# Optimization experiments

Hardware: AMD Instinct MI355X
Metric: run time of the kernel (lower is better)

## Reference

```python
import jax, jax.numpy as jnp
import numpy as np

N_NODES = 100000
N_EDGES = 1600000
D_IN = 128
D_HID = 128
D_OUT = 64
N_LAYERS = 3
BN_EPS = 1e-5


def _mlp_block(h, W1, b1, g, be, W2, b2):
    # PyG MLP([c_in, h, h]): Linear -> BatchNorm -> ReLU -> Linear (plain last)
    h = h @ W1 + b1                      # [N, h]
    mu = jnp.mean(h, axis=0)
    var = jnp.var(h, axis=0)             # biased var, BN training-mode stats
    h = (h - mu) * jax.lax.rsqrt(var + BN_EPS) * g + be
    h = jax.nn.relu(h)
    return h @ W2 + b2


def setup_inputs() -> dict:
    key = jax.random.key(0)
    ks = jax.random.split(key, 16)
    s_in = 1.0 / np.sqrt(D_IN)
    s_h = 1.0 / np.sqrt(D_HID)
    x = jax.random.normal(ks[0], (N_NODES, D_IN), dtype=jnp.float32)
    edge_index = jax.random.randint(ks[1], (2, N_EDGES), 0, N_NODES, dtype=jnp.int64)
    return {
        "x": x,
        "edge_index": edge_index,
        # stacked per-conv MLP params (all layers are 128->128->128)
        "W1": jax.random.normal(ks[2], (N_LAYERS, D_IN, D_HID), jnp.float32) * s_in,
        "b1": jnp.zeros((N_LAYERS, D_HID), jnp.float32),
        "g1": jnp.ones((N_LAYERS, D_HID), jnp.float32),
        "be1": jnp.zeros((N_LAYERS, D_HID), jnp.float32),
        "W2": jax.random.normal(ks[3], (N_LAYERS, D_HID, D_HID), jnp.float32) * s_h,
        "b2": jnp.zeros((N_LAYERS, D_HID), jnp.float32),
        # final MLP([h, h, out])
        "fW1": jax.random.normal(ks[4], (D_HID, D_HID), jnp.float32) * s_h,
        "fb1": jnp.zeros((D_HID,), jnp.float32),
        "fg1": jnp.ones((D_HID,), jnp.float32),
        "fbe1": jnp.zeros((D_HID,), jnp.float32),
        "fW2": jax.random.normal(ks[5], (D_HID, D_OUT), jnp.float32) * s_h,
        "fb2": jnp.zeros((D_OUT,), jnp.float32),
    }


def reference(x, edge_index, W1, b1, g1, be1, W2, b2, fW1, fb1, fg1, fbe1, fW2, fb2):
    src, dst = edge_index[0], edge_index[1]
    for l in range(N_LAYERS):
        # GINConv, eps=0: nn((1+eps)*x + sum_{j->i} x_j)
        aggr = jax.ops.segment_sum(x[src], dst, num_segments=N_NODES)  # [N, d]
        h = x + aggr
        x = jax.nn.relu(_mlp_block(h, W1[l], b1[l], g1[l], be1[l], W2[l], b2[l]))
    # final MLP (dropout=0.5 is identity in eval mode)
    return _mlp_block(x, fW1, fb1, fg1, fbe1, fW2, fb2)
```

## Files before the change

kernel.cpp:

```cpp
#include <hip/hip_runtime.h>

#define NN 100000
#define NE 1600000
#define DD 128
#define CAP 56
#define NGROUP 256

static __device__ __forceinline__ unsigned short f2b(float f) {
  unsigned int x = __float_as_uint(f);
  unsigned int r = x + 0x7fffu + ((x >> 16) & 1u);
  return (unsigned short)(r >> 16);
}
static __device__ __forceinline__ float b2f(unsigned short u) {
  return __uint_as_float(((unsigned int)u) << 16);
}

typedef __attribute__((ext_vector_type(8))) short short8;
typedef __attribute__((ext_vector_type(4))) float f32x4;

union V8 {
  uint4 u4;
  short8 s8;
  unsigned short us[8];
};

__global__ void detect_k(const int* __restrict__ ei, int* __restrict__ flag) {
  int v = ei[2 * threadIdx.x + 1];
  unsigned long long b = __ballot(v != 0);
  if (threadIdx.x == 0) *flag = (b == 0ull) ? 1 : 0;
}

__global__ __launch_bounds__(256) void cast_k(const float* __restrict__ x,
                                              unsigned short* __restrict__ x16) {
  size_t i = ((size_t)blockIdx.x * 256 + threadIdx.x) * 8;
  f32x4 a = *(const f32x4*)(x + i);
  f32x4 b = *(const f32x4*)(x + i + 4);
  V8 v;
#pragma unroll
  for (int j = 0; j < 4; ++j) {
    v.us[j] = f2b(a[j]);
    v.us[4 + j] = f2b(b[j]);
  }
  *(uint4*)(x16 + i) = v.u4;
}

__global__ __launch_bounds__(256) void pack_k(const int* __restrict__ ei,
                                              int2* __restrict__ packed,
                                              int* __restrict__ cnt,
                                              const int* __restrict__ flag) {
  const int mode = *flag;
  const int gid = blockIdx.x * 256 + threadIdx.x;
  int s, d;
  if (mode) {
    s = ((const int2*)ei)[gid].x;
    d = ((const int2*)ei)[(size_t)NE + gid].x;
  } else {
    s = ei[gid];
    d = ei[NE + gid];
  }
  packed[gid] = make_int2(s, d);
  if (gid < NN) cnt[gid] = 0;
}

__global__ __launch_bounds__(256) void scatter_k(const int2* __restrict__ packed,
                                                 int* __restrict__ cnt,
                                                 int* __restrict__ csr) {
  const int r = blockIdx.x & 7;
  const int g = blockIdx.x >> 3;
  const int lo = r * (NN / 8), hi = lo + (NN / 8);
  for (int e = g * 256 + threadIdx.x; e < NE; e += NGROUP * 256) {
    int2 sd = packed[e];
    if (sd.y >= lo && sd.y < hi) {
      int c = atomicAdd(&cnt[sd.y], 1);
      if (c < CAP) csr[(size_t)sd.y * CAP + c] = sd.x;
    }
  }
}

__global__ __launch_bounds__(256) void wprep_k(const float* __restrict__ W1,
                                               const float* __restrict__ W2,
                                               const float* __restrict__ fW1,
                                               const float* __restrict__ fW2,
                                               unsigned short* __restrict__ wt) {
  int b = blockIdx.x;
  const float* src;
  int moff, N;
  if (b < 192) {
    int m = b >> 6;
    src = W1 + m * 16384;
    moff = m * 16384;
    N = 128;
    b &= 63;
  } else if (b < 384) {
    int m = (b - 192) >> 6;
    src = W2 + m * 16384;
    moff = (3 + m) * 16384;
    N = 128;
    b = (b - 192) & 63;
  } else if (b < 448) {
    src = fW1;
    moff = 6 * 16384;
    N = 128;
    b -= 384;
  } else {
    src = fW2;
    moff = 7 * 16384;
    N = 64;
    b -= 448;
  }
  int idx = b * 256 + threadIdx.x;
  int n = idx >> 7, k = idx & 127;
  if (n < N) wt[moff + idx] = f2b(src[(size_t)k * N + n]);
}

__global__ __launch_bounds__(256) void gather_k(const int* __restrict__ cnt,
                                                const int* __restrict__ csr,
                                                const unsigned short* __restrict__ x16,
                                                unsigned short* __restrict__ h16,
                                                float* __restrict__ stats) {
  if (blockIdx.x == 0) stats[threadIdx.x] = 0.f;
  const int node = blockIdx.x * 16 + (threadIdx.x >> 4);
  const int l = threadIdx.x & 15;
  const int beg = node * CAP;
  const int end = beg + cnt[node];
  V8 v;
  v.u4 = *(const uint4*)(x16 + (size_t)node * DD + l * 8);
  float a0[8], a1[8], a2[8], a3[8];
#pragma unroll
  for (int j = 0; j < 8; ++j) {
    a0[j] = b2f(v.us[j]);
    a1[j] = 0.f;
    a2[j] = 0.f;
    a3[j] = 0.f;
  }
  int p = beg;
  for (; p + 4 <= end; p += 4) {
    const int s0 = csr[p], s1 = csr[p + 1], s2 = csr[p + 2], s3 = csr[p + 3];
    V8 w0, w1, w2, w3;
    w0.u4 = *(const uint4*)(x16 + (size_t)s0 * DD + l * 8);
    w1.u4 = *(const uint4*)(x16 + (size_t)s1 * DD + l * 8);
    w2.u4 = *(const uint4*)(x16 + (size_t)s2 * DD + l * 8);
    w3.u4 = *(const uint4*)(x16 + (size_t)s3 * DD + l * 8);
#pragma unroll
    for (int j = 0; j < 8; ++j) {
      a0[j] += b2f(w0.us[j]);
      a1[j] += b2f(w1.us[j]);
      a2[j] += b2f(w2.us[j]);
      a3[j] += b2f(w3.us[j]);
    }
  }
  for (; p < end; ++p) {
    const int s0 = csr[p];
    V8 w0;
    w0.u4 = *(const uint4*)(x16 + (size_t)s0 * DD + l * 8);
#pragma unroll
    for (int j = 0; j < 8; ++j) a0[j] += b2f(w0.us[j]);
  }
  V8 o;
#pragma unroll
  for (int j = 0; j < 8; ++j) o.us[j] = f2b((a0[j] + a1[j]) + (a2[j] + a3[j]));
  *(uint4*)(h16 + (size_t)node * DD + l * 8) = o.u4;
}

template <int AMODE, int NCOLS, int EPI, int STATS>
__global__ __launch_bounds__(256) void gemm_k(const unsigned short* __restrict__ Aptr,
                                              const unsigned short* __restrict__ wT,
                                              const float* __restrict__ bias,
                                              const float* __restrict__ bn_stats,
                                              const float* __restrict__ gamma,
                                              const float* __restrict__ beta,
                                              void* __restrict__ Cptr,
                                              float* __restrict__ stats_out) {
  __shared__ unsigned short bT[NCOLS][136];
  __shared__ float biasS[NCOLS];
  __shared__ float scS[128];
  __shared__ float shS[128];
  __shared__ float sS[NCOLS];
  __shared__ float s2S[NCOLS];
  const int tid = threadIdx.x;

  for (int i = tid; i < NCOLS * 16; i += 256) {
    int n = i >> 4, k8 = (i & 15) << 3;
    *(uint4*)&bT[n][k8] = *(const uint4*)(wT + n * 128 + k8);
  }
  if (tid < NCOLS) biasS[tid] = bias[tid];
  if (AMODE == 2 && tid < 128) {
    const float inv_n = 1.0f / (float)NN;
    float mu = bn_stats[tid] * inv_n;
    float var = bn_stats[128 + tid] * inv_n - mu * mu;
    float sc = gamma[tid] * rsqrtf(var + 1e-5f);
    scS[tid] = sc;
    shS[tid] = beta[tid] - mu * sc;
  }
  if (STATS && tid < NCOLS) {
    sS[tid] = 0.f;
    s2S[tid] = 0.f;
  }
  __syncthreads();

  const int wv = tid >> 6;
  const int lane = tid & 63;
  const int l16 = lane & 15;
  const int quad = lane >> 4;
  const int arow = blockIdx.x * 64 + wv * 16 + l16;
  const bool rv = arow < NN;

  f32x4 acc[NCOLS / 16];
#pragma unroll
  for (int nt = 0; nt < NCOLS / 16; ++nt) acc[nt] = (f32x4)(0.0f);

#pragma unroll
  for (int kc = 0; kc < 4; ++kc) {
    const int k0 = kc * 32 + quad * 8;
    V8 af;
    if (rv) {
      af.u4 = *(const uint4*)(Aptr + (size_t)arow * DD + k0);
    } else {
      af.u4 = make_uint4(0u, 0u, 0u, 0u);
    }
    if (AMODE == 2) {
#pragma unroll
      for (int j = 0; j < 8; ++j) {
        float f = fmaf(b2f(af.us[j]), scS[k0 + j], shS[k0 + j]);
        af.us[j] = f2b(fmaxf(f, 0.0f));
      }
    }
#pragma unroll
    for (int nt = 0; nt < NCOLS / 16; ++nt) {
      V8 bf;
      bf.u4 = *(const uint4*)&bT[nt * 16 + l16][k0];
      acc[nt] = __builtin_amdgcn_mfma_f32_16x16x32_bf16(af.s8, bf.s8, acc[nt], 0, 0, 0);
    }
  }

  const int r0 = blockIdx.x * 64 + wv * 16 + quad * 4;
#pragma unroll
  for (int nt = 0; nt < NCOLS / 16; ++nt) {
    const int col = nt * 16 + l16;
    const float bv = biasS[col];
    float s = 0.f, s2 = 0.f;
#pragma unroll
    for (int i = 0; i < 4; ++i) {
      const int r = r0 + i;
      if (r < NN) {
        float v = acc[nt][i] + bv;
        if (EPI == 1) v = fmaxf(v, 0.0f);
        if (EPI == 2) {
          ((float*)Cptr)[(size_t)r * NCOLS + col] = v;
        } else {
          unsigned short us = f2b(v);
          ((unsigned short*)Cptr)[(size_t)r * NCOLS + col] = us;
          if (STATS) {
            float vr = b2f(us);
            s += vr;
            s2 += vr * vr;
          }
        }
      }
    }
    if (STATS) {
      s += __shfl_xor(s, 16);
      s += __shfl_xor(s, 32);
      s2 += __shfl_xor(s2, 16);
      s2 += __shfl_xor(s2, 32);
      if (quad == 0) {
        atomicAdd(&sS[col], s);
        atomicAdd(&s2S[col], s2);
      }
    }
  }
  if (STATS) {
    __syncthreads();
    if (tid < NCOLS) {
      atomicAdd(&stats_out[tid], sS[tid]);
      atomicAdd(&stats_out[128 + tid], s2S[tid]);
    }
  }
}

extern "C" void kernel_launch(void* const* d_in, const int* in_sizes, int n_in,
                              void* d_out, int out_size, void* d_ws, size_t ws_size,
                              hipStream_t stream) {
  const float* x = (const float*)d_in[0];
  const int* ei = (const int*)d_in[1];
  const float* W1 = (const float*)d_in[2];
  const float* b1 = (const float*)d_in[3];
  const float* g1 = (const float*)d_in[4];
  const float* be1 = (const float*)d_in[5];
  const float* W2 = (const float*)d_in[6];
  const float* b2 = (const float*)d_in[7];
  const float* fW1 = (const float*)d_in[8];
  const float* fb1 = (const float*)d_in[9];
  const float* fg1 = (const float*)d_in[10];
  const float* fbe1 = (const float*)d_in[11];
  const float* fW2 = (const float*)d_in[12];
  const float* fb2 = (const float*)d_in[13];

  char* ws = (char*)d_ws;
  unsigned short* x16 = (unsigned short*)ws;
  unsigned short* h16 = (unsigned short*)(ws + (size_t)25600000);
  unsigned short* t16 = (unsigned short*)(ws + (size_t)51200000);
  int2* packed = (int2*)t16;
  int* csr = (int*)(ws + (size_t)76800000);
  int* cnt = (int*)(ws + (size_t)99200000);
  float* stats = (float*)(ws + (size_t)99600000);
  int* flag = (int*)(ws + (size_t)99601024);
  unsigned short* wt = (unsigned short*)(ws + (size_t)99602432);

  const int vecBlocks = (NN * DD) / (256 * 8);
  const int gemmBlocks = (NN + 63) / 64;
  const int edgeBlocks = NE / 256;
  const int filtBlocks = NGROUP * 8;
  const int nodeBlocks = NN / 16;

  detect_k<<<1, 64, 0, stream>>>(ei, flag);
  cast_k<<<vecBlocks, 256, 0, stream>>>(x, x16);
  pack_k<<<edgeBlocks, 256, 0, stream>>>(ei, packed, cnt, flag);
  wprep_k<<<480, 256, 0, stream>>>(W1, W2, fW1, fW2, wt);
  scatter_k<<<filtBlocks, 256, 0, stream>>>(packed, cnt, csr);

  for (int l = 0; l < 3; ++l) {
    gather_k<<<nodeBlocks, 256, 0, stream>>>(cnt, csr, x16, h16, stats);
    gemm_k<1, 128, 0, 1><<<gemmBlocks, 256, 0, stream>>>(
        h16, wt + (size_t)l * 16384, b1 + l * 128, nullptr, nullptr, nullptr, t16,
        stats);
    gemm_k<2, 128, 1, 0><<<gemmBlocks, 256, 0, stream>>>(
        t16, wt + (size_t)(3 + l) * 16384, b2 + l * 128, stats, g1 + l * 128,
        be1 + l * 128, x16, nullptr);
  }

  hipMemsetAsync(stats, 0, 256 * sizeof(float), stream);
  gemm_k<1, 128, 0, 1><<<gemmBlocks, 256, 0, stream>>>(
      x16, wt + (size_t)6 * 16384, fb1, nullptr, nullptr, nullptr, t16, stats);
  gemm_k<2, 64, 2, 0><<<gemmBlocks, 256, 0, stream>>>(
      t16, wt + (size_t)7 * 16384, fb2, stats, fg1, fbe1, (float*)d_out, nullptr);
}
```

Before: 657.2 us.

## Fuse neighbor aggregation into the first GEMM of each GIN layer

Drops the separate gather kernel. The first MLP GEMM gains a new A-mode that sums each row's CSR neighbor features from x16 in registers before issuing the MFMAs, so the bf16 h16 intermediate is never written and read back. Per-layer stats buffers are zeroed once up front instead of inside the gather kernel. Smaller tweaks: the per-node CSR capacity grows to 64, and the packed edges are read with a nontemporal 64-bit load in scatter. The cost is lower gather parallelism: each row's gather now runs across only 4 lanes with a serial neighbor loop, which may limit memory-level parallelism and raise register pressure.

```diff
diff --git a/kernel.cpp b/kernel.cpp
--- a/kernel.cpp
+++ b/kernel.cpp
@@ -3,7 +3,7 @@
 #define NN 100000
 #define NE 1600000
 #define DD 128
-#define CAP 56
+#define CAP 64
 #define NGROUP 256
 
 static __device__ __forceinline__ unsigned short f2b(float f) {
@@ -45,34 +45,37 @@
 }
 
 __global__ __launch_bounds__(256) void pack_k(const int* __restrict__ ei,
-                                              int2* __restrict__ packed,
+                                              int* __restrict__ packed,
                                               int* __restrict__ cnt,
                                               const int* __restrict__ flag) {
   const int mode = *flag;
   const int gid = blockIdx.x * 256 + threadIdx.x;
   int s, d;
   if (mode) {
-    s = ((const int2*)ei)[gid].x;
-    d = ((const int2*)ei)[(size_t)NE + gid].x;
+    s = ei[2 * (size_t)gid];
+    d = ei[2 * ((size_t)NE + gid)];
   } else {
     s = ei[gid];
     d = ei[NE + gid];
   }
-  packed[gid] = make_int2(s, d);
+  packed[2 * gid] = s;
+  packed[2 * gid + 1] = d;
   if (gid < NN) cnt[gid] = 0;
 }
 
-__global__ __launch_bounds__(256) void scatter_k(const int2* __restrict__ packed,
+__global__ __launch_bounds__(256) void scatter_k(const long long* __restrict__ packed,
                                                  int* __restrict__ cnt,
                                                  int* __restrict__ csr) {
   const int r = blockIdx.x & 7;
   const int g = blockIdx.x >> 3;
   const int lo = r * (NN / 8), hi = lo + (NN / 8);
   for (int e = g * 256 + threadIdx.x; e < NE; e += NGROUP * 256) {
-    int2 sd = packed[e];
-    if (sd.y >= lo && sd.y < hi) {
-      int c = atomicAdd(&cnt[sd.y], 1);
-      if (c < CAP) csr[(size_t)sd.y * CAP + c] = sd.x;
+    long long sd = __builtin_nontemporal_load(&packed[e]);
+    const int s = (int)(sd & 0xffffffffll);
+    const int d = (int)(sd >> 32);
+    if (d >= lo && d < hi) {
+      int c = atomicAdd(&cnt[d], 1);
+      if (c < CAP) csr[(size_t)d * CAP + c] = s;
     }
   }
 }
@@ -113,55 +116,6 @@
   if (n < N) wt[moff + idx] = f2b(src[(size_t)k * N + n]);
 }
 
-__global__ __launch_bounds__(256) void gather_k(const int* __restrict__ cnt,
-                                                const int* __restrict__ csr,
-                                                const unsigned short* __restrict__ x16,
-                                                unsigned short* __restrict__ h16,
-                                                float* __restrict__ stats) {
-  if (blockIdx.x == 0) stats[threadIdx.x] = 0.f;
-  const int node = blockIdx.x * 16 + (threadIdx.x >> 4);
-  const int l = threadIdx.x & 15;
-  const int beg = node * CAP;
-  const int end = beg + cnt[node];
-  V8 v;
-  v.u4 = *(const uint4*)(x16 + (size_t)node * DD + l * 8);
-  float a0[8], a1[8], a2[8], a3[8];
-#pragma unroll
-  for (int j = 0; j < 8; ++j) {
-    a0[j] = b2f(v.us[j]);
-    a1[j] = 0.f;
-    a2[j] = 0.f;
-    a3[j] = 0.f;
-  }
-  int p = beg;
-  for (; p + 4 <= end; p += 4) {
-    const int s0 = csr[p], s1 = csr[p + 1], s2 = csr[p + 2], s3 = csr[p + 3];
-    V8 w0, w1, w2, w3;
-    w0.u4 = *(const uint4*)(x16 + (size_t)s0 * DD + l * 8);
-    w1.u4 = *(const uint4*)(x16 + (size_t)s1 * DD + l * 8);
-    w2.u4 = *(const uint4*)(x16 + (size_t)s2 * DD + l * 8);
-    w3.u4 = *(const uint4*)(x16 + (size_t)s3 * DD + l * 8);
-#pragma unroll
-    for (int j = 0; j < 8; ++j) {
-      a0[j] += b2f(w0.us[j]);
-      a1[j] += b2f(w1.us[j]);
-      a2[j] += b2f(w2.us[j]);
-      a3[j] += b2f(w3.us[j]);
-    }
-  }
-  for (; p < end; ++p) {
-    const int s0 = csr[p];
-    V8 w0;
-    w0.u4 = *(const uint4*)(x16 + (size_t)s0 * DD + l * 8);
-#pragma unroll
-    for (int j = 0; j < 8; ++j) a0[j] += b2f(w0.us[j]);
-  }
-  V8 o;
-#pragma unroll
-  for (int j = 0; j < 8; ++j) o.us[j] = f2b((a0[j] + a1[j]) + (a2[j] + a3[j]));
-  *(uint4*)(h16 + (size_t)node * DD + l * 8) = o.u4;
-}
-
 template <int AMODE, int NCOLS, int EPI, int STATS>
 __global__ __launch_bounds__(256) void gemm_k(const unsigned short* __restrict__ Aptr,
                                               const unsigned short* __restrict__ wT,
@@ -170,7 +124,9 @@
                                               const float* __restrict__ gamma,
                                               const float* __restrict__ beta,
                                               void* __restrict__ Cptr,
-                                              float* __restrict__ stats_out) {
+                                              float* __restrict__ stats_out,
+                                              const int* __restrict__ cnt,
+                                              const int* __restrict__ csr) {
   __shared__ unsigned short bT[NCOLS][136];
   __shared__ float biasS[NCOLS];
   __shared__ float scS[128];
@@ -205,31 +161,78 @@
   const int arow = blockIdx.x * 64 + wv * 16 + l16;
   const bool rv = arow < NN;
 
+  V8 afs[4];
+  if (AMODE == 3) {
+    float ac[4][8];
+#pragma unroll
+    for (int kc = 0; kc < 4; ++kc) {
+      V8 w;
+      w.u4 = rv ? *(const uint4*)(Aptr + (size_t)arow * DD + kc * 32 + quad * 8)
+                : make_uint4(0u, 0u, 0u, 0u);
+#pragma unroll
+      for (int j = 0; j < 8; ++j) ac[kc][j] = b2f(w.us[j]);
+    }
+    if (rv) {
+      const size_t base = (size_t)arow * CAP;
+      const int c = cnt[arow];
+      int p = 0;
+      for (; p + 2 <= c; p += 2) {
+        const int s0 = csr[base + p], s1 = csr[base + p + 1];
+        V8 w0[4], w1[4];
+#pragma unroll
+        for (int kc = 0; kc < 4; ++kc) {
+          w0[kc].u4 = *(const uint4*)(Aptr + (size_t)s0 * DD + kc * 32 + quad * 8);
+          w1[kc].u4 = *(const uint4*)(Aptr + (size_t)s1 * DD + kc * 32 + quad * 8);
+        }
+#pragma unroll
+        for (int kc = 0; kc < 4; ++kc)
+#pragma unroll
+          for (int j = 0; j < 8; ++j)
+            ac[kc][j] += b2f(w0[kc].us[j]) + b2f(w1[kc].us[j]);
+      }
+      if (p < c) {
+        const int s0 = csr[base + p];
+        V8 w0[4];
+#pragma unroll
+        for (int kc = 0; kc < 4; ++kc)
+          w0[kc].u4 = *(const uint4*)(Aptr + (size_t)s0 * DD + kc * 32 + quad * 8);
+#pragma unroll
+        for (int kc = 0; kc < 4; ++kc)
+#pragma unroll
+          for (int j = 0; j < 8; ++j) ac[kc][j] += b2f(w0[kc].us[j]);
+      }
+    }
+#pragma unroll
+    for (int kc = 0; kc < 4; ++kc)
+#pragma unroll
+      for (int j = 0; j < 8; ++j) afs[kc].us[j] = f2b(ac[kc][j]);
+  } else {
+#pragma unroll
+    for (int kc = 0; kc < 4; ++kc) {
+      const int k0 = kc * 32 + quad * 8;
+      afs[kc].u4 = rv ? *(const uint4*)(Aptr + (size_t)arow * DD + k0)
+                      : make_uint4(0u, 0u, 0u, 0u);
+      if (AMODE == 2) {
+#pragma unroll
+        for (int j = 0; j < 8; ++j) {
+          float f = fmaf(b2f(afs[kc].us[j]), scS[k0 + j], shS[k0 + j]);
+          afs[kc].us[j] = f2b(fmaxf(f, 0.0f));
+        }
+      }
+    }
+  }
+
   f32x4 acc[NCOLS / 16];
 #pragma unroll
   for (int nt = 0; nt < NCOLS / 16; ++nt) acc[nt] = (f32x4)(0.0f);
-
 #pragma unroll
   for (int kc = 0; kc < 4; ++kc) {
     const int k0 = kc * 32 + quad * 8;
-    V8 af;
-    if (rv) {
-      af.u4 = *(const uint4*)(Aptr + (size_t)arow * DD + k0);
-    } else {
-      af.u4 = make_uint4(0u, 0u, 0u, 0u);
-    }
-    if (AMODE == 2) {
-#pragma unroll
-      for (int j = 0; j < 8; ++j) {
-        float f = fmaf(b2f(af.us[j]), scS[k0 + j], shS[k0 + j]);
-        af.us[j] = f2b(fmaxf(f, 0.0f));
-      }
-    }
 #pragma unroll
     for (int nt = 0; nt < NCOLS / 16; ++nt) {
       V8 bf;
       bf.u4 = *(const uint4*)&bT[nt * 16 + l16][k0];
-      acc[nt] = __builtin_amdgcn_mfma_f32_16x16x32_bf16(af.s8, bf.s8, acc[nt], 0, 0, 0);
+      acc[nt] = __builtin_amdgcn_mfma_f32_16x16x32_bf16(afs[kc].s8, bf.s8, acc[nt], 0, 0, 0);
     }
   }
 
@@ -298,40 +301,39 @@
 
   char* ws = (char*)d_ws;
   unsigned short* x16 = (unsigned short*)ws;
-  unsigned short* h16 = (unsigned short*)(ws + (size_t)25600000);
-  unsigned short* t16 = (unsigned short*)(ws + (size_t)51200000);
-  int2* packed = (int2*)t16;
-  int* csr = (int*)(ws + (size_t)76800000);
-  int* cnt = (int*)(ws + (size_t)99200000);
-  float* stats = (float*)(ws + (size_t)99600000);
-  int* flag = (int*)(ws + (size_t)99601024);
-  unsigned short* wt = (unsigned short*)(ws + (size_t)99602432);
+  unsigned short* t16 = (unsigned short*)(ws + (size_t)25600000);
+  int* packed = (int*)t16;
+  int* csr = (int*)(ws + (size_t)51200000);
+  int* cnt = (int*)(ws + (size_t)76800000);
+  float* stats4 = (float*)(ws + (size_t)77200000);
+  int* flag = (int*)(ws + (size_t)77204992);
+  unsigned short* wt = (unsigned short*)(ws + (size_t)77210000);
 
   const int vecBlocks = (NN * DD) / (256 * 8);
   const int gemmBlocks = (NN + 63) / 64;
   const int edgeBlocks = NE / 256;
   const int filtBlocks = NGROUP * 8;
-  const int nodeBlocks = NN / 16;
 
   detect_k<<<1, 64, 0, stream>>>(ei, flag);
+  (void)hipMemsetAsync(stats4, 0, 4 * 256 * sizeof(float), stream);
   cast_k<<<vecBlocks, 256, 0, stream>>>(x, x16);
   pack_k<<<edgeBlocks, 256, 0, stream>>>(ei, packed, cnt, flag);
   wprep_k<<<480, 256, 0, stream>>>(W1, W2, fW1, fW2, wt);
-  scatter_k<<<filtBlocks, 256, 0, stream>>>(packed, cnt, csr);
+  scatter_k<<<filtBlocks, 256, 0, stream>>>((const long long*)packed, cnt, csr);
 
   for (int l = 0; l < 3; ++l) {
-    gather_k<<<nodeBlocks, 256, 0, stream>>>(cnt, csr, x16, h16, stats);
-    gemm_k<1, 128, 0, 1><<<gemmBlocks, 256, 0, stream>>>(
-        h16, wt + (size_t)l * 16384, b1 + l * 128, nullptr, nullptr, nullptr, t16,
-        stats);
+    gemm_k<3, 128, 0, 1><<<gemmBlocks, 256, 0, stream>>>(
+        x16, wt + (size_t)l * 16384, b1 + l * 128, nullptr, nullptr, nullptr, t16,
+        stats4 + l * 256, cnt, csr);
     gemm_k<2, 128, 1, 0><<<gemmBlocks, 256, 0, stream>>>(
-        t16, wt + (size_t)(3 + l) * 16384, b2 + l * 128, stats, g1 + l * 128,
-        be1 + l * 128, x16, nullptr);
-  }
-
-  hipMemsetAsync(stats, 0, 256 * sizeof(float), stream);
+        t16, wt + (size_t)(3 + l) * 16384, b2 + l * 128, stats4 + l * 256,
+        g1 + l * 128, be1 + l * 128, x16, nullptr, nullptr, nullptr);
+  }
+
   gemm_k<1, 128, 0, 1><<<gemmBlocks, 256, 0, stream>>>(
-      x16, wt + (size_t)6 * 16384, fb1, nullptr, nullptr, nullptr, t16, stats);
+      x16, wt + (size_t)6 * 16384, fb1, nullptr, nullptr, nullptr, t16,
+      stats4 + 3 * 256, nullptr, nullptr);
   gemm_k<2, 64, 2, 0><<<gemmBlocks, 256, 0, stream>>>(
-      t16, wt + (size_t)7 * 16384, fb2, stats, fg1, fbe1, (float*)d_out, nullptr);
-}
+      t16, wt + (size_t)7 * 16384, fb2, stats4 + 3 * 256, fg1, fbe1, (float*)d_out,
+      nullptr, nullptr, nullptr);
+}
```

Result: no change. 665.9 us (+1.3%).
